# Kernel optimization log

Hardware: AMD Instinct MI355X
Metric: run time of the kernel (lower is better)

## Reference

```python
import jax, jax.numpy as jnp
import numpy as np

B, N, C = 8, 4096, 512
NH, R = 8, 4
EPS = 1e-5

def setup_inputs() -> dict:
    key = jax.random.key(0)
    ks = jax.random.split(key, 6)
    s = lambda k, shape: jax.random.normal(k, shape, jnp.float32) * 0.02
    return {
        'x': jax.random.normal(ks[0], (B, N, C), jnp.float32),
        'Wq': s(ks[1], (C, C)), 'bq': jnp.zeros((C,), jnp.float32),
        'Wkv': s(ks[2], (C, 2 * C)), 'bkv': jnp.zeros((2 * C,), jnp.float32),
        'Wp': s(ks[3], (C, C)), 'bp': jnp.zeros((C,), jnp.float32),
        'Wsr': s(ks[4], (C, C, R, R)), 'bsr': jnp.zeros((C,), jnp.float32),
        'gamma': jnp.ones((C,), jnp.float32), 'beta': jnp.zeros((C,), jnp.float32),
        'H': 64, 'W': 64,
    }

def reference(x, Wq, bq, Wkv, bkv, Wp, bp, Wsr, bsr, gamma, beta, H, W):
    b, n, c = x.shape
    nh = NH
    hd = c // nh
    scale = hd ** -0.5
    # Q projection -> [B, nh, N, hd]
    q = (x @ Wq + bq).reshape(b, n, nh, hd).transpose(0, 2, 1, 3)
    # spatial reduction of KV input: Conv2d(k=stride=R), NCHW
    x_sp = x.transpose(0, 2, 1).reshape(b, c, H, W)
    xr = jax.lax.conv_general_dilated(
        x_sp, Wsr, window_strides=(R, R), padding='VALID',
        dimension_numbers=('NCHW', 'OIHW', 'NCHW')) + bsr[None, :, None, None]
    nr = (H // R) * (W // R)
    xr = xr.reshape(b, c, nr).transpose(0, 2, 1)  # [B, Nr, C]
    # LayerNorm over channels
    mu = xr.mean(-1, keepdims=True)
    var = xr.var(-1, keepdims=True)
    xr = (xr - mu) / jnp.sqrt(var + EPS) * gamma + beta
    # KV projection -> k, v: [B, nh, Nr, hd]
    kv = (xr @ Wkv + bkv).reshape(b, nr, 2, nh, hd)
    k = kv[:, :, 0].transpose(0, 2, 1, 3)
    v = kv[:, :, 1].transpose(0, 2, 1, 3)
    # attention
    attn = jax.nn.softmax(jnp.einsum('bhnd,bhmd->bhnm', q, k) * scale, axis=-1)
    out = jnp.einsum('bhnm,bhmd->bhnd', attn, v).transpose(0, 2, 1, 3).reshape(b, n, c)
    return out @ Wp + bp
```

## Files before the change

### kernel.cpp

```cpp
#include <hip/hip_runtime.h>
#include <stdint.h>

typedef __attribute__((ext_vector_type(8))) short bf16x8;
typedef __attribute__((ext_vector_type(4))) float f32x4;
typedef __attribute__((ext_vector_type(2))) unsigned u32x2;

#define MFMA16(a,b,c) __builtin_amdgcn_mfma_f32_16x16x32_bf16(a,b,c,0,0,0)

typedef const __attribute__((address_space(1))) void GV;
typedef __attribute__((address_space(3))) void LV;

static __device__ __forceinline__ void gload16(const void* g, void* l) {
  __builtin_amdgcn_global_load_lds((GV*)g, (LV*)l, 16, 0, 0);
}

static __device__ __forceinline__ unsigned short f2bf(float f) {
  union { float f; unsigned u; } x; x.f = f;
  unsigned r = x.u + 0x7FFFu + ((x.u >> 16) & 1u);
  return (unsigned short)(r >> 16);
}

static __device__ __forceinline__ float fast_exp2(float x) {
#if __has_builtin(__builtin_amdgcn_exp2f)
  return __builtin_amdgcn_exp2f(x);
#else
  return __expf(x * 0.6931471805599453f);
#endif
}

__global__ __launch_bounds__(256) void pack_all(
    const float* __restrict__ x, const float* __restrict__ Wq,
    const float* __restrict__ Wkv, const float* __restrict__ Wp,
    const float* __restrict__ Wsr,
    unsigned short* __restrict__ xb, unsigned short* __restrict__ wqt,
    unsigned short* __restrict__ wkvt, unsigned short* __restrict__ wpt,
    unsigned short* __restrict__ wsrt) {
  const int tid = threadIdx.x;
  int bid = blockIdx.x;
  if (bid < 16384) {
    int i = bid * 256 + tid;
    float4 v = ((const float4*)x)[i];
    unsigned a0 = f2bf(v.x), a1 = f2bf(v.y), a2 = f2bf(v.z), a3 = f2bf(v.w);
    uint2 pk; pk.x = a0 | (a1 << 16); pk.y = a2 | (a3 << 16);
    ((uint2*)xb)[i] = pk;
    return;
  }
  bid -= 16384;
  __shared__ float lsm[8704];

  auto wtile = [&](const float* __restrict__ W, unsigned short* __restrict__ out,
                   int ldw, int tr, int tc) {
    int k0 = tr * 64, n0 = tc * 64;
    #pragma unroll
    for (int i = 0; i < 16; ++i) {
      int idx = i * 256 + tid; int r = idx >> 6, c = idx & 63;
      lsm[r * 65 + c] = W[(size_t)(k0 + r) * ldw + n0 + c];
    }
    __syncthreads();
    #pragma unroll
    for (int i = 0; i < 16; ++i) {
      int idx = i * 256 + tid; int n = idx >> 6, k = idx & 63;
      out[(size_t)(n0 + n) * 512 + k0 + k] = f2bf(lsm[k * 65 + n]);
    }
  };

  if (bid < 64) { wtile(Wq, wqt, 512, bid >> 3, bid & 7); return; }
  bid -= 64;
  if (bid < 128) { wtile(Wkv, wkvt, 1024, bid >> 4, bid & 15); return; }
  bid -= 128;
  if (bid < 64) { wtile(Wp, wpt, 512, bid >> 3, bid & 7); return; }
  bid -= 64;
  int oc = bid;
  #pragma unroll
  for (int i = 0; i < 32; ++i) {
    int idx = i * 256 + tid;
    lsm[(idx >> 4) * 17 + (idx & 15)] = Wsr[(size_t)oc * 8192 + idx];
  }
  __syncthreads();
  #pragma unroll
  for (int i = 0; i < 32; ++i) {
    int idx = i * 256 + tid;
    int ic = idx & 511, r12 = idx >> 9;
    wsrt[(size_t)oc * 8192 + idx] = f2bf(lsm[ic * 17 + r12]);
  }
}

template<int MODE, bool CONV>
static __device__ __forceinline__ void gemm8_body(
    unsigned short* lds_a, unsigned short* lds_b,
    const unsigned short* __restrict__ A, const unsigned short* __restrict__ Bt,
    const float* __restrict__ bias, void* __restrict__ outp,
    unsigned short* __restrict__ out_k, unsigned short* __restrict__ out_v,
    int M, int N, int K, int lda, int Ksub, int m0, int n0, int kbeg, int zslice) {
  constexpr int BK = 64;
  constexpr int ABYTES = 128 * BK * 2;
  const int tid = threadIdx.x;
  const int lane = tid & 63, w = tid >> 6;
  const int wr = w >> 2, wc = w & 3;
  const int l15 = lane & 15, lhi = lane >> 4;
  const int xmask = (l15 & 7) << 4;
  const int smask = ((tid >> 3) & 7) << 3;

  f32x4 acc[4][2] = {};

  auto stage = [&](int buf, int k0) {
    #pragma unroll
    for (int r = 0; r < 2; ++r) {
      int o = r * 8192 + tid * 16;
      int row = o >> 7;
      int kc = (((o & 127) >> 1)) ^ smask;
      const unsigned short* src;
      if constexpr (CONV) {
        int m = m0 + row;
        int bb = m >> 8, pix = m & 255;
        int oh = pix >> 4, ow = pix & 15;
        int r12 = k0 >> 9;
        int icc = (k0 & 511) + kc;
        int r1 = r12 >> 2, r2 = r12 & 3;
        int nn = (oh * 4 + r1) * 64 + ow * 4 + r2;
        src = A + ((size_t)(bb * 4096 + nn)) * 512 + icc;
      } else {
        src = A + (size_t)(m0 + row) * lda + k0 + kc;
      }
      gload16(src, (char*)lds_a + buf * ABYTES + r * 8192 + w * 1024);
    }
    #pragma unroll
    for (int r = 0; r < 2; ++r) {
      int o = r * 8192 + tid * 16;
      int row = o >> 7;
      int kc = (((o & 127) >> 1)) ^ smask;
      const unsigned short* src = Bt + (size_t)(n0 + row) * K + k0 + kc;
      gload16(src, (char*)lds_b + buf * ABYTES + r * 8192 + w * 1024);
    }
  };

  auto compute = [&](int buf) {
    const char* pa = (const char*)lds_a + buf * ABYTES;
    const char* pb = (const char*)lds_b + buf * ABYTES;
    #pragma unroll
    for (int kk = 0; kk < BK; kk += 32) {
      bf16x8 af[4], bfr[2];
      #pragma unroll
      for (int m = 0; m < 4; ++m)
        af[m] = *(const bf16x8*)(pa + (wr * 64 + m * 16 + l15) * 128
                                 + (((kk << 1) + (lhi << 4)) ^ xmask));
      #pragma unroll
      for (int n = 0; n < 2; ++n)
        bfr[n] = *(const bf16x8*)(pb + (wc * 32 + n * 16 + l15) * 128
                                  + (((kk << 1) + (lhi << 4)) ^ xmask));
      __builtin_amdgcn_s_setprio(1);
      #pragma unroll
      for (int m = 0; m < 4; ++m)
        #pragma unroll
        for (int n = 0; n < 2; ++n)
          acc[m][n] = MFMA16(af[m], bfr[n], acc[m][n]);
      __builtin_amdgcn_s_setprio(0);
    }
  };

  const int nsteps = Ksub / BK;
  stage(0, kbeg);
  int buf = 0;
  for (int t = 0; t < nsteps; ++t) {
    if (t + 1 < nsteps) {
      stage(buf ^ 1, kbeg + (t + 1) * BK);
      asm volatile("s_waitcnt vmcnt(4)" ::: "memory");
    } else {
      asm volatile("s_waitcnt vmcnt(0)" ::: "memory");
    }
    __builtin_amdgcn_s_barrier();
    compute(buf);
    __builtin_amdgcn_s_barrier();
    buf ^= 1;
  }

  #pragma unroll
  for (int m = 0; m < 4; ++m) {
    #pragma unroll
    for (int n = 0; n < 2; ++n) {
      #pragma unroll
      for (int r = 0; r < 4; ++r) {
        int gm = m0 + wr * 64 + m * 16 + lhi * 4 + r;
        int gn = n0 + wc * 32 + n * 16 + l15;
        if constexpr (MODE == 0) {
          ((float*)outp)[(size_t)gm * N + gn] = acc[m][n][r] + bias[gn];
        } else if constexpr (MODE == 3) {
          ((float*)outp)[((size_t)zslice * M + gm) * N + gn] = acc[m][n][r];
        } else if constexpr (MODE == 4) {
          float v = (acc[m][n][r] + bias[gn]) * 0.18033688011112042f;
          int b_ = gm >> 12, n_ = gm & 4095;
          int hh = gn >> 6, d = gn & 63;
          int qt = n_ >> 4, half = d >> 5, dd = d & 31;
          int ln = (n_ & 15) | ((dd >> 3) << 4);
          ((unsigned short*)outp)[(size_t)(b_ * 8 + hh) * 262144 +
              (qt * 2 + half) * 512 + ln * 8 + (d & 7)] = f2bf(v);
        } else {
          float v = acc[m][n][r] + bias[gn];
          unsigned short bv = f2bf(v);
          int bb = gm >> 8, nr = gm & 255;
          if (gn < 512) {
            int hh = gn >> 6, d = gn & 63;
            int t_ = nr >> 4, half = d >> 5, dd = d & 31;
            int ln = (nr & 15) | ((dd >> 3) << 4);
            out_k[(size_t)(bb * 8 + hh) * 16384 +
                  (t_ * 2 + half) * 512 + ln * 8 + (d & 7)] = bv;
          } else {
            int c = gn - 512;
            int hh = c >> 6, d = c & 63;
            int nn = d >> 4, cl = d & 15;
            int ks = nr >> 5, lh = (nr >> 3) & 3;
            out_v[(size_t)(bb * 8 + hh) * 16384 +
                  (nn * 8 + ks) * 512 + (cl | (lh << 4)) * 8 + (nr & 7)] = bv;
          }
        }
      }
    }
  }
}

template<int MODE, bool CONV, bool SWZ>
__global__ __launch_bounds__(512, 4) void gemm8(
    const unsigned short* __restrict__ A, const unsigned short* __restrict__ Bt,
    const float* __restrict__ bias, void* __restrict__ outp,
    unsigned short* __restrict__ out_k, unsigned short* __restrict__ out_v,
    int M, int N, int K, int lda, int Ksub) {
  __shared__ unsigned short lds_a[2 * 128 * 64];
  __shared__ unsigned short lds_b[2 * 128 * 64];
  int mt, nt_;
  if constexpr (SWZ) {
    int lin = blockIdx.x + blockIdx.y * gridDim.x;
    int nwg = gridDim.x * gridDim.y;
    int cpx = nwg >> 3;
    int s = (lin & 7) * cpx + (lin >> 3);
    int gdy = gridDim.y;
    mt = s / gdy; nt_ = s - mt * gdy;
  } else { mt = blockIdx.x; nt_ = blockIdx.y; }
  gemm8_body<MODE, CONV>(lds_a, lds_b, A, Bt, bias, outp, out_k, out_v,
                         M, N, K, lda, Ksub, mt * 128, nt_ * 128,
                         blockIdx.z * Ksub, blockIdx.z);
}

__global__ __launch_bounds__(512, 4) void proj_fused(
    const unsigned short* __restrict__ xb, const unsigned short* __restrict__ wqt,
    const float* __restrict__ bq, unsigned short* __restrict__ qfrag,
    const unsigned short* __restrict__ xln, const unsigned short* __restrict__ wkvt,
    const float* __restrict__ bkv, unsigned short* __restrict__ kfrag,
    unsigned short* __restrict__ vfrag) {
  __shared__ unsigned short lds_a[2 * 128 * 64];
  __shared__ unsigned short lds_b[2 * 128 * 64];
  int bx = blockIdx.x;
  if (bx < 1024) {
    int s = (bx & 7) * 128 + (bx >> 3);
    int mt = s >> 2, nt_ = s & 3;
    gemm8_body<4, false>(lds_a, lds_b, xb, wqt, bq, qfrag, nullptr, nullptr,
                         32768, 512, 512, 512, 512, mt * 128, nt_ * 128, 0, 0);
  } else {
    int b2 = bx - 1024;
    int mt = b2 >> 3, nt_ = b2 & 7;
    gemm8_body<2, false>(lds_a, lds_b, xln, wkvt, bkv, nullptr, kfrag, vfrag,
                         2048, 1024, 512, 512, 512, mt * 128, nt_ * 128, 0, 0);
  }
}

__global__ __launch_bounds__(64) void ln_kernel(
    const float* __restrict__ part, const float* __restrict__ bsr,
    const float* __restrict__ gamma, const float* __restrict__ beta,
    unsigned short* __restrict__ xln) {
  const int row = blockIdx.x, lane = threadIdx.x;
  float vv[8];
  #pragma unroll
  for (int j = 0; j < 8; ++j) vv[j] = bsr[lane * 8 + j];
  #pragma unroll
  for (int p = 0; p < 8; ++p) {
    const float* pp = part + ((size_t)p * 2048 + row) * 512 + lane * 8;
    float4 a0 = *(const float4*)pp;
    float4 a1 = *(const float4*)(pp + 4);
    vv[0] += a0.x; vv[1] += a0.y; vv[2] += a0.z; vv[3] += a0.w;
    vv[4] += a1.x; vv[5] += a1.y; vv[6] += a1.z; vv[7] += a1.w;
  }
  float s = 0.f, s2 = 0.f;
  #pragma unroll
  for (int j = 0; j < 8; ++j) { s += vv[j]; s2 += vv[j] * vv[j]; }
  #pragma unroll
  for (int m_ = 1; m_ < 64; m_ <<= 1) { s += __shfl_xor(s, m_); s2 += __shfl_xor(s2, m_); }
  float mean = s * (1.f / 512.f);
  float var = s2 * (1.f / 512.f) - mean * mean;
  float inv = rsqrtf(var + 1e-5f);
  #pragma unroll
  for (int j = 0; j < 8; ++j) {
    int c = lane * 8 + j;
    xln[(size_t)row * 512 + c] = f2bf((vv[j] - mean) * inv * gamma[c] + beta[c]);
  }
}

__global__ __launch_bounds__(512, 4) void attn_kernel(
    const unsigned short* __restrict__ qfrag, const unsigned short* __restrict__ kfrag,
    const unsigned short* __restrict__ vfrag, unsigned short* __restrict__ aout) {
  __shared__ unsigned short k_lds[16384];
  __shared__ unsigned short v_lds[16384];
  const int tid = threadIdx.x, lane = tid & 63, w = tid >> 6;
  const int l15 = lane & 15;
  const int b = blockIdx.z, h = blockIdx.y;
  const int bh = b * 8 + h;
  const char* kb_ = (const char*)(kfrag + (size_t)bh * 16384);
  const char* vb_ = (const char*)(vfrag + (size_t)bh * 16384);
  #pragma unroll
  for (int r = 0; r < 4; ++r) {
    gload16(kb_ + r * 8192 + tid * 16, (char*)k_lds + r * 8192 + w * 1024);
    gload16(vb_ + r * 8192 + tid * 16, (char*)v_lds + r * 8192 + w * 1024);
  }
  const int qt = blockIdx.x * 8 + w;
  const unsigned short* qbase = qfrag + (size_t)bh * 262144 + (size_t)qt * 1024;
  bf16x8 qf0 = *(const bf16x8*)(qbase + lane * 8);
  bf16x8 qf1 = *(const bf16x8*)(qbase + 512 + lane * 8);
  __syncthreads();

  f32x4 st[16];
  #pragma unroll
  for (int t = 0; t < 16; ++t) {
    bf16x8 kf0 = *(const bf16x8*)&k_lds[t * 1024 + lane * 8];
    bf16x8 kf1 = *(const bf16x8*)&k_lds[t * 1024 + 512 + lane * 8];
    f32x4 a = {0.f, 0.f, 0.f, 0.f};
    a = MFMA16(kf0, qf0, a);
    a = MFMA16(kf1, qf1, a);
    st[t] = a;
  }

  float sum = 0.f;
  unsigned pk2[16][2];
  #pragma unroll
  for (int t = 0; t < 16; ++t) {
    float p0 = fast_exp2(st[t][0]), p1 = fast_exp2(st[t][1]);
    float p2 = fast_exp2(st[t][2]), p3 = fast_exp2(st[t][3]);
    sum += (p0 + p1) + (p2 + p3);
    unsigned r0, r1;
    asm("v_cvt_pk_bf16_f32 %0, %1, %2" : "=v"(r0) : "v"(p0), "v"(p1));
    asm("v_cvt_pk_bf16_f32 %0, %1, %2" : "=v"(r1) : "v"(p2), "v"(p3));
    pk2[t][0] = r0; pk2[t][1] = r1;
  }
  sum += __shfl_xor(sum, 16);
  sum += __shfl_xor(sum, 32);
  float invs = 1.f / sum;

  const int lhi_ = lane >> 4;
  const int srcA = l15 + (((2 * lhi_) & 3) << 4);
  const int srcB = l15 + (((2 * lhi_ + 1) & 3) << 4);
  const bool hi2 = lhi_ >= 2;
  f32x4 o[4] = {};
  #pragma unroll
  for (int ks = 0; ks < 8; ++ks) {
    union { unsigned u[4]; bf16x8 v; } pu;
    unsigned A0 = __shfl(pk2[2 * ks][0], srcA),     A0b = __shfl(pk2[2 * ks][1], srcA);
    unsigned A1 = __shfl(pk2[2 * ks + 1][0], srcA), A1b = __shfl(pk2[2 * ks + 1][1], srcA);
    unsigned B0 = __shfl(pk2[2 * ks][0], srcB),     B0b = __shfl(pk2[2 * ks][1], srcB);
    unsigned B1 = __shfl(pk2[2 * ks + 1][0], srcB), B1b = __shfl(pk2[2 * ks + 1][1], srcB);
    pu.u[0] = hi2 ? A1 : A0;  pu.u[1] = hi2 ? A1b : A0b;
    pu.u[2] = hi2 ? B1 : B0;  pu.u[3] = hi2 ? B1b : B0b;
    #pragma unroll
    for (int n = 0; n < 4; ++n) {
      bf16x8 vf = *(const bf16x8*)&v_lds[(n * 8 + ks) * 512 + lane * 8];
      o[n] = MFMA16(vf, pu.v, o[n]);
    }
  }

  const int q0 = blockIdx.x * 128;
  const int lhi = lane >> 4;
  #pragma unroll
  for (int n = 0; n < 4; ++n) {
    float a0 = o[n][0] * invs, a1 = o[n][1] * invs;
    float a2 = o[n][2] * invs, a3 = o[n][3] * invs;
    unsigned w0, w1;
    asm("v_cvt_pk_bf16_f32 %0, %1, %2" : "=v"(w0) : "v"(a0), "v"(a1));
    asm("v_cvt_pk_bf16_f32 %0, %1, %2" : "=v"(w1) : "v"(a2), "v"(a3));
    u32x2 pr; pr[0] = w0; pr[1] = w1;
    size_t base = (size_t)(b * 4096 + q0 + w * 16 + l15) * 512 + h * 64 + n * 16 + lhi * 4;
    *(u32x2*)(aout + base) = pr;
  }
}

extern "C" void kernel_launch(void* const* d_in, const int* in_sizes, int n_in,
                              void* d_out, int out_size, void* d_ws, size_t ws_size,
                              hipStream_t stream) {
  const float* x     = (const float*)d_in[0];
  const float* Wq    = (const float*)d_in[1];
  const float* bq    = (const float*)d_in[2];
  const float* Wkv   = (const float*)d_in[3];
  const float* bkv   = (const float*)d_in[4];
  const float* Wp    = (const float*)d_in[5];
  const float* bp    = (const float*)d_in[6];
  const float* Wsr   = (const float*)d_in[7];
  const float* bsr   = (const float*)d_in[8];
  const float* gamma = (const float*)d_in[9];
  const float* beta  = (const float*)d_in[10];

  char* ws = (char*)d_ws;
  unsigned short* xb    = (unsigned short*)(ws + 0);
  float*          part  = (float*)(ws + 33554432);
  unsigned short* qfrag = (unsigned short*)(ws + 33554432);
  unsigned short* wqt   = (unsigned short*)(ws + 67108864);
  unsigned short* wkvt  = (unsigned short*)(ws + 67633152);
  unsigned short* wpt   = (unsigned short*)(ws + 68681728);
  unsigned short* wsrt  = (unsigned short*)(ws + 69206016);
  unsigned short* xln   = (unsigned short*)(ws + 77594624);
  unsigned short* kfrag = (unsigned short*)(ws + 79691776);
  unsigned short* vfrag = (unsigned short*)(ws + 81788928);
  unsigned short* aout  = xb;

  pack_all<<<17152, 256, 0, stream>>>(x, Wq, Wkv, Wp, Wsr, xb, wqt, wkvt, wpt, wsrt);
  gemm8<3, true, true><<<dim3(16, 4, 8), 512, 0, stream>>>(
      xb, wsrt, nullptr, part, nullptr, nullptr, 2048, 512, 8192, 512, 1024);
  ln_kernel<<<2048, 64, 0, stream>>>(part, bsr, gamma, beta, xln);
  proj_fused<<<1152, 512, 0, stream>>>(xb, wqt, bq, qfrag, xln, wkvt, bkv, kfrag, vfrag);
  attn_kernel<<<dim3(32, 8, 8), 512, 0, stream>>>(qfrag, kfrag, vfrag, aout);
  gemm8<0, false, true><<<dim3(256, 4, 1), 512, 0, stream>>>(
      aout, wpt, bp, (float*)d_out, nullptr, nullptr, 32768, 512, 512, 512, 512);
}
```

Before: 151.7 us.

## Fuse conv-reduction GEMM with Q projection when workspace permits

Adds a convq_fused kernel that runs the strided-conv split-K GEMM and the Q projection GEMM in one launch. This needs qfrag and part to stop aliasing, so it only runs when the workspace is at least 120MB; the KV projection then becomes its own launch after LayerNorm. LayerNorm now packs four rows per 256-thread block instead of one row per 64-thread block. The intent is to fill the GPU better during the small conv GEMM and cut launch overhead. In exchange the KV GEMM runs as a separate small launch, and the new path depends on workspace size.

```diff
diff --git a/kernel.cpp b/kernel.cpp
--- a/kernel.cpp
+++ b/kernel.cpp
@@ -240,6 +240,29 @@
                          blockIdx.z * Ksub, blockIdx.z);
 }
 
+__global__ __launch_bounds__(512, 4) void convq_fused(
+    const unsigned short* __restrict__ xb, const unsigned short* __restrict__ wsrt,
+    float* __restrict__ part,
+    const unsigned short* __restrict__ wqt, const float* __restrict__ bq,
+    unsigned short* __restrict__ qfrag) {
+  __shared__ unsigned short lds_a[2 * 128 * 64];
+  __shared__ unsigned short lds_b[2 * 128 * 64];
+  int bx = blockIdx.x;
+  if (bx < 512) {
+    int z = bx >> 6, rem = bx & 63;
+    int mt = rem >> 2, nt_ = rem & 3;
+    gemm8_body<3, true>(lds_a, lds_b, xb, wsrt, nullptr, part, nullptr, nullptr,
+                        2048, 512, 8192, 512, 1024, mt * 128, nt_ * 128,
+                        z * 1024, z);
+  } else {
+    int b2 = bx - 512;
+    int s = (b2 & 7) * 128 + (b2 >> 3);
+    int mt = s >> 2, nt_ = s & 3;
+    gemm8_body<4, false>(lds_a, lds_b, xb, wqt, bq, qfrag, nullptr, nullptr,
+                         32768, 512, 512, 512, 512, mt * 128, nt_ * 128, 0, 0);
+  }
+}
+
 __global__ __launch_bounds__(512, 4) void proj_fused(
     const unsigned short* __restrict__ xb, const unsigned short* __restrict__ wqt,
     const float* __restrict__ bq, unsigned short* __restrict__ qfrag,
@@ -262,11 +285,12 @@
   }
 }
 
-__global__ __launch_bounds__(64) void ln_kernel(
+__global__ __launch_bounds__(256) void ln_kernel(
     const float* __restrict__ part, const float* __restrict__ bsr,
     const float* __restrict__ gamma, const float* __restrict__ beta,
     unsigned short* __restrict__ xln) {
-  const int row = blockIdx.x, lane = threadIdx.x;
+  const int row = blockIdx.x * 4 + (threadIdx.x >> 6);
+  const int lane = threadIdx.x & 63;
   float vv[8];
   #pragma unroll
   for (int j = 0; j < 8; ++j) vv[j] = bsr[lane * 8 + j];
@@ -394,24 +418,49 @@
   const float* beta  = (const float*)d_in[10];
 
   char* ws = (char*)d_ws;
-  unsigned short* xb    = (unsigned short*)(ws + 0);
-  float*          part  = (float*)(ws + 33554432);
-  unsigned short* qfrag = (unsigned short*)(ws + 33554432);
-  unsigned short* wqt   = (unsigned short*)(ws + 67108864);
-  unsigned short* wkvt  = (unsigned short*)(ws + 67633152);
-  unsigned short* wpt   = (unsigned short*)(ws + 68681728);
-  unsigned short* wsrt  = (unsigned short*)(ws + 69206016);
-  unsigned short* xln   = (unsigned short*)(ws + 77594624);
-  unsigned short* kfrag = (unsigned short*)(ws + 79691776);
-  unsigned short* vfrag = (unsigned short*)(ws + 81788928);
-  unsigned short* aout  = xb;
-
-  pack_all<<<17152, 256, 0, stream>>>(x, Wq, Wkv, Wp, Wsr, xb, wqt, wkvt, wpt, wsrt);
-  gemm8<3, true, true><<<dim3(16, 4, 8), 512, 0, stream>>>(
-      xb, wsrt, nullptr, part, nullptr, nullptr, 2048, 512, 8192, 512, 1024);
-  ln_kernel<<<2048, 64, 0, stream>>>(part, bsr, gamma, beta, xln);
-  proj_fused<<<1152, 512, 0, stream>>>(xb, wqt, bq, qfrag, xln, wkvt, bkv, kfrag, vfrag);
-  attn_kernel<<<dim3(32, 8, 8), 512, 0, stream>>>(qfrag, kfrag, vfrag, aout);
-  gemm8<0, false, true><<<dim3(256, 4, 1), 512, 0, stream>>>(
-      aout, wpt, bp, (float*)d_out, nullptr, nullptr, 32768, 512, 512, 512, 512);
-}
+  const bool big = ws_size >= (size_t)120 * 1024 * 1024;
+
+  if (big) {
+    unsigned short* xb    = (unsigned short*)(ws + 0);
+    float*          part  = (float*)(ws + 33554432);
+    unsigned short* qfrag = (unsigned short*)(ws + 67108864);
+    unsigned short* wqt   = (unsigned short*)(ws + 100663296);
+    unsigned short* wkvt  = (unsigned short*)(ws + 101187584);
+    unsigned short* wpt   = (unsigned short*)(ws + 102236160);
+    unsigned short* wsrt  = (unsigned short*)(ws + 102760448);
+    unsigned short* xln   = (unsigned short*)(ws + 111149056);
+    unsigned short* kfrag = (unsigned short*)(ws + 113246208);
+    unsigned short* vfrag = (unsigned short*)(ws + 115343360);
+    unsigned short* aout  = xb;
+
+    pack_all<<<17152, 256, 0, stream>>>(x, Wq, Wkv, Wp, Wsr, xb, wqt, wkvt, wpt, wsrt);
+    convq_fused<<<1536, 512, 0, stream>>>(xb, wsrt, part, wqt, bq, qfrag);
+    ln_kernel<<<512, 256, 0, stream>>>(part, bsr, gamma, beta, xln);
+    gemm8<2, false, false><<<dim3(16, 8), 512, 0, stream>>>(
+        xln, wkvt, bkv, nullptr, kfrag, vfrag, 2048, 1024, 512, 512, 512);
+    attn_kernel<<<dim3(32, 8, 8), 512, 0, stream>>>(qfrag, kfrag, vfrag, aout);
+    gemm8<0, false, true><<<dim3(256, 4, 1), 512, 0, stream>>>(
+        aout, wpt, bp, (float*)d_out, nullptr, nullptr, 32768, 512, 512, 512, 512);
+  } else {
+    unsigned short* xb    = (unsigned short*)(ws + 0);
+    float*          part  = (float*)(ws + 33554432);
+    unsigned short* qfrag = (unsigned short*)(ws + 33554432);
+    unsigned short* wqt   = (unsigned short*)(ws + 67108864);
+    unsigned short* wkvt  = (unsigned short*)(ws + 67633152);
+    unsigned short* wpt   = (unsigned short*)(ws + 68681728);
+    unsigned short* wsrt  = (unsigned short*)(ws + 69206016);
+    unsigned short* xln   = (unsigned short*)(ws + 77594624);
+    unsigned short* kfrag = (unsigned short*)(ws + 79691776);
+    unsigned short* vfrag = (unsigned short*)(ws + 81788928);
+    unsigned short* aout  = xb;
+
+    pack_all<<<17152, 256, 0, stream>>>(x, Wq, Wkv, Wp, Wsr, xb, wqt, wkvt, wpt, wsrt);
+    gemm8<3, true, true><<<dim3(16, 4, 8), 512, 0, stream>>>(
+        xb, wsrt, nullptr, part, nullptr, nullptr, 2048, 512, 8192, 512, 1024);
+    ln_kernel<<<512, 256, 0, stream>>>(part, bsr, gamma, beta, xln);
+    proj_fused<<<1152, 512, 0, stream>>>(xb, wqt, bq, qfrag, xln, wkvt, bkv, kfrag, vfrag);
+    attn_kernel<<<dim3(32, 8, 8), 512, 0, stream>>>(qfrag, kfrag, vfrag, aout);
+    gemm8<0, false, true><<<dim3(256, 4, 1), 512, 0, stream>>>(
+        aout, wpt, bp, (float*)d_out, nullptr, nullptr, 32768, 512, 512, 512, 512);
+  }
+}
```

New measurement: 161.1 us. 1.06x slower.
